# Kernel tuning notes

Measured on AMD Instinct MI355X. Metric: run time of the kernel, lower is better.

## Reference

```python
import jax, jax.numpy as jnp
import numpy as np

B, S, D = 2, 2048, 3584
H, KV, HD = 28, 4, 128
N_REP = H // KV          # 7
MAX_S = 2048
SCALE = HD ** -0.5
ROPE_BASE = 1_000_000.0  # Qwen2 rope theta


def _rope_tables(max_s, hd, base):
    inv = 1.0 / (base ** (np.arange(0, hd, 2, dtype=np.float32) / hd))  # [hd/2]
    ang = np.arange(max_s, dtype=np.float32)[:, None] * inv[None, :]    # [S, hd/2]
    return jnp.asarray(np.cos(ang)), jnp.asarray(np.sin(ang))


def apply_rotary(x, cos, sin):
    # x: [b, s, h, hd] with interleaved complex pairs (torch view_as_complex layout)
    xr = x[..., 0::2]
    xi = x[..., 1::2]
    cos = cos[None, :, None, :]
    sin = sin[None, :, None, :]
    yr = xr * cos - xi * sin
    yi = xr * sin + xi * cos
    return jnp.stack([yr, yi], axis=-1).reshape(x.shape)


def setup_inputs() -> dict:
    key = jax.random.key(0)
    ks = jax.random.split(key, 8)
    w = 0.02
    x = jax.random.normal(ks[0], (B, S, D), jnp.float32)
    wq_w = jax.random.normal(ks[1], (H * HD, D), jnp.float32) * w
    wq_b = jax.random.normal(ks[2], (H * HD,), jnp.float32) * w
    wk_w = jax.random.normal(ks[3], (KV * HD, D), jnp.float32) * w
    wk_b = jax.random.normal(ks[4], (KV * HD,), jnp.float32) * w
    wv_w = jax.random.normal(ks[5], (KV * HD, D), jnp.float32) * w
    wv_b = jax.random.normal(ks[6], (KV * HD,), jnp.float32) * w
    wo_w = jax.random.normal(ks[7], (D, H * HD), jnp.float32) * w
    k_cache = jnp.zeros((B, MAX_S, KV, HD), jnp.float32)
    v_cache = jnp.zeros((B, MAX_S, KV, HD), jnp.float32)
    freqs_cos, freqs_sin = _rope_tables(MAX_S, HD, ROPE_BASE)
    # causal additive mask [s, t]; large-negative instead of -inf for safe grads
    mask = jnp.triu(jnp.full((S, S), -1e9, jnp.float32), k=1)
    return {"x": x, "wq_w": wq_w, "wq_b": wq_b, "wk_w": wk_w, "wk_b": wk_b,
            "wv_w": wv_w, "wv_b": wv_b, "wo_w": wo_w,
            "k_cache": k_cache, "v_cache": v_cache,
            "freqs_cos": freqs_cos, "freqs_sin": freqs_sin,
            "mask": mask, "start_pos": 0}


def reference(x, wq_w, wq_b, wk_w, wk_b, wv_w, wv_b, wo_w,
              k_cache, v_cache, freqs_cos, freqs_sin, mask, start_pos):
    bsz, seqlen, _ = x.shape
    end_pos = start_pos + seqlen
    q = (x @ wq_w.T + wq_b).reshape(bsz, seqlen, H, HD)
    k = (x @ wk_w.T + wk_b).reshape(bsz, seqlen, KV, HD)
    v = (x @ wv_w.T + wv_b).reshape(bsz, seqlen, KV, HD)
    cos = jax.lax.dynamic_slice_in_dim(freqs_cos, start_pos, seqlen, 0)
    sin = jax.lax.dynamic_slice_in_dim(freqs_sin, start_pos, seqlen, 0)
    q = apply_rotary(q, cos, sin)
    k = apply_rotary(k, cos, sin)
    # KV-cache write
    k_cache = jax.lax.dynamic_update_slice(k_cache, k, (0, start_pos, 0, 0))
    v_cache = jax.lax.dynamic_update_slice(v_cache, v, (0, start_pos, 0, 0))
    keys = k_cache[:bsz, :end_pos]    # [b, t, kv, hd]
    values = v_cache[:bsz, :end_pos]
    # GQA: repeat_interleave kv heads to n_heads
    keys = jnp.repeat(keys, N_REP, axis=2)      # [b, t, h, hd]
    values = jnp.repeat(values, N_REP, axis=2)
    scores = jnp.einsum('bshd,bthd->bsht', q, keys) * SCALE
    scores = scores + mask[None, :, None, :]
    probs = jax.nn.softmax(scores.astype(jnp.float32), axis=-1).astype(x.dtype)
    out = jnp.einsum('bsht,bthd->bshd', probs, values)
    out = out.reshape(bsz, seqlen, H * HD)
    return out @ wo_w.T
```

## Files before the change

kernel.cpp:

```cpp
#include <hip/hip_runtime.h>
#include <hip/hip_bf16.h>

typedef __attribute__((ext_vector_type(4)))  float  f32x4;
typedef __attribute__((ext_vector_type(16))) float  f32x16;
typedef __attribute__((ext_vector_type(8)))  __bf16 bf16x8;
typedef __attribute__((ext_vector_type(4)))  __bf16 bf16x4;
typedef __attribute__((ext_vector_type(4)))  unsigned int u32x4;

constexpr int S_LEN = 2048, DMODEL = 3584, NH = 28, NKV = 4, HD = 128, NREP = 7;
constexpr float SCALE_LOG2 = 0.1275174331f;

__device__ __forceinline__ unsigned int pack2(float a, float b) {
  unsigned short ua = __builtin_bit_cast(unsigned short, (__bf16)a);
  unsigned short ub = __builtin_bit_cast(unsigned short, (__bf16)b);
  return (unsigned int)ua | ((unsigned int)ub << 16);
}

__global__ void cvt5_kernel(const float* __restrict__ s0, const float* __restrict__ s1,
                            const float* __restrict__ s2, const float* __restrict__ s3,
                            const float* __restrict__ s4,
                            __bf16* __restrict__ d0, __bf16* __restrict__ d1,
                            __bf16* __restrict__ d2, __bf16* __restrict__ d3,
                            __bf16* __restrict__ d4,
                            int n0, int n1, int n2, int n3, int* __restrict__ ctr, int total) {
  if (blockIdx.x == 0 && threadIdx.x == 0) *ctr = 0;
  for (int i = blockIdx.x * blockDim.x + threadIdx.x; i < total; i += gridDim.x * blockDim.x) {
    const float* s; __bf16* d; int j = i;
    if (j < n0) { s = s0; d = d0; }
    else { j -= n0;
      if (j < n1) { s = s1; d = d1; }
      else { j -= n1;
        if (j < n2) { s = s2; d = d2; }
        else { j -= n2;
          if (j < n3) { s = s3; d = d3; }
          else { j -= n3; s = s4; d = d4; }
        }
      }
    }
    float4 v = reinterpret_cast<const float4*>(s)[j];
    bf16x4 o;
    o[0] = (__bf16)v.x; o[1] = (__bf16)v.y; o[2] = (__bf16)v.z; o[3] = (__bf16)v.w;
    reinterpret_cast<bf16x4*>(d)[j] = o;
  }
}

#define GLDS16(gsrc, ldst)                                                              \
  __builtin_amdgcn_global_load_lds((const __attribute__((address_space(1))) void*)(gsrc),\
                                   (__attribute__((address_space(3))) void*)(ldst), 16, 0, 0)

template <int MODE>
__global__ __launch_bounds__(512, 2) void gemm256(
    const __bf16* __restrict__ A, const __bf16* __restrict__ Bw,
    const float* __restrict__ bias, void* __restrict__ Cout,
    int M, int N, int K,
    const float* __restrict__ fcos, const float* __restrict__ fsin,
    const int* __restrict__ sp_ptr, float scale)
{
  extern __shared__ char smem[];
  const int tid = threadIdx.x;
  const int lane = tid & 63, wid = tid >> 6;
  const int wm = wid >> 2, wn = wid & 3;
  const int l15 = lane & 15, g = (lane >> 4) & 3;

  const int chunk = gridDim.x >> 3;
  const int wg = (blockIdx.x & 7) * chunk + (blockIdx.x >> 3);
  const int nbx = N >> 8;
  const int by = wg / nbx, bx = wg % nbx;
  const int row0 = by * 256, col0 = bx * 256;

  const int srL   = 16 * (tid >> 6) + ((tid >> 2) & 15);
  const int cperm = ((tid & 3) * 8) ^ (((tid >> 5) & 1) * 16);
  const __bf16* pA0 = A + (size_t)(row0 + srL) * K + cperm;
  const __bf16* pA1 = pA0 + (size_t)128 * K;
  const __bf16* pB0 = Bw + (size_t)(col0 + srL) * K + cperm;
  const __bf16* pB1 = pB0 + (size_t)128 * K;
  char* ldsA = smem + tid * 16;
  char* ldsB = smem + 65536 + tid * 16;

  const int sw = ((l15 >> 3) & 1) << 5;
  const int aoff = wm * 8192 + l15 * 64 + ((g * 16) ^ sw);
  const int boff = 65536 + wn * 4096 + l15 * 64 + ((g * 16) ^ sw);

  f32x4 acc[8][4] = {};
  const int nt = K >> 5;

#pragma unroll
  for (int pt = 0; pt < 3; pt++) {
    const size_t ko = (size_t)pt * 32;
    char* sA = ldsA + pt * 16384;
    char* sB = ldsB + pt * 16384;
    GLDS16(pA0 + ko, sA);
    GLDS16(pA1 + ko, sA + 8192);
    GLDS16(pB0 + ko, sB);
    GLDS16(pB1 + ko, sB + 8192);
  }
  asm volatile("s_waitcnt vmcnt(8)" ::: "memory");
  __builtin_amdgcn_s_barrier();
  __builtin_amdgcn_sched_barrier(0);

  for (int t = 0; t < nt; t++) {
    const int slot = (t & 3) * 16384;
    const char* sa = smem + slot + aoff;
    const char* sb = smem + slot + boff;
    bf16x8 a0[4], a1[4], bfv[4];

#pragma unroll
    for (int fn = 0; fn < 4; fn++)
      bfv[fn] = *reinterpret_cast<const bf16x8*>(sb + fn * 1024);
#pragma unroll
    for (int fm = 0; fm < 4; fm++)
      a0[fm] = *reinterpret_cast<const bf16x8*>(sa + fm * 1024);
#pragma unroll
    for (int fm = 0; fm < 4; fm++)
      a1[fm] = *reinterpret_cast<const bf16x8*>(sa + (4 + fm) * 1024);

    if (t + 3 < nt) {
      const size_t ko = (size_t)(t + 3) * 32;
      char* sA = ldsA + ((t + 3) & 3) * 16384;
      char* sB = ldsB + ((t + 3) & 3) * 16384;
      GLDS16(pA0 + ko, sA);
      GLDS16(pA1 + ko, sA + 8192);
      GLDS16(pB0 + ko, sB);
      GLDS16(pB1 + ko, sB + 8192);
    }

    asm volatile("s_waitcnt lgkmcnt(4)" ::: "memory");
    __builtin_amdgcn_sched_barrier(0);
    __builtin_amdgcn_s_setprio(1);
#pragma unroll
    for (int fn = 0; fn < 4; fn++)
#pragma unroll
      for (int fm = 0; fm < 4; fm++)
        acc[fm][fn] = __builtin_amdgcn_mfma_f32_16x16x32_bf16(a0[fm], bfv[fn], acc[fm][fn], 0, 0, 0);
    __builtin_amdgcn_s_setprio(0);

    asm volatile("s_waitcnt lgkmcnt(0)" ::: "memory");
    __builtin_amdgcn_sched_barrier(0);
    __builtin_amdgcn_s_setprio(1);
#pragma unroll
    for (int fn = 0; fn < 4; fn++)
#pragma unroll
      for (int fm = 0; fm < 4; fm++)
        acc[4 + fm][fn] = __builtin_amdgcn_mfma_f32_16x16x32_bf16(a1[fm], bfv[fn], acc[4 + fm][fn], 0, 0, 0);
    __builtin_amdgcn_s_setprio(0);

    if (t < nt - 3)       asm volatile("s_waitcnt vmcnt(8)" ::: "memory");
    else if (t == nt - 3) asm volatile("s_waitcnt vmcnt(4)" ::: "memory");
    else if (t == nt - 2) asm volatile("s_waitcnt vmcnt(0)" ::: "memory");
    __builtin_amdgcn_s_barrier();
    __builtin_amdgcn_sched_barrier(0);
  }

  if constexpr (MODE == 0) {
    float* C = (float*)Cout;
#pragma unroll
    for (int fm = 0; fm < 8; fm++) {
      const int row = row0 + wm * 128 + fm * 16 + 4 * g;
#pragma unroll
      for (int fn = 0; fn < 4; fn++) {
        const int col = col0 + wn * 64 + fn * 16 + l15;
#pragma unroll
        for (int r = 0; r < 4; r++)
          C[(size_t)(row + r) * N + col] = acc[fm][fn][r];
      }
    }
  } else {
    __bf16* C = (__bf16*)Cout;
    const int sp = sp_ptr[0];
    float bval[4];
#pragma unroll
    for (int fn = 0; fn < 4; fn++) bval[fn] = bias[col0 + wn * 64 + fn * 16 + l15];
#pragma unroll
    for (int fm = 0; fm < 8; fm++) {
#pragma unroll
      for (int fn = 0; fn < 4; fn++) {
        const int col = col0 + wn * 64 + fn * 16 + l15;
        const int i = (col & (HD - 1)) >> 1;
#pragma unroll
        for (int r = 0; r < 4; r++) {
          const int row = row0 + wm * 128 + fm * 16 + 4 * g + r;
          float y = acc[fm][fn][r] + bval[fn];
          float p = __shfl_xor(y, 1);
          const int spos = sp + (row & (S_LEN - 1));
          const float c = fcos[spos * (HD / 2) + i];
          const float sn = fsin[spos * (HD / 2) + i];
          y = (col & 1) ? (p * sn + y * c) : (y * c - p * sn);
          C[(size_t)row * N + col] = (__bf16)(y * scale);
        }
      }
    }
  }
}

__global__ __launch_bounds__(256) void gemm_kv(
    const __bf16* __restrict__ A,
    const __bf16* __restrict__ Wk, const float* __restrict__ bk, __bf16* __restrict__ Ko,
    const __bf16* __restrict__ Wv, const float* __restrict__ bv, __bf16* __restrict__ Vo,
    const float* __restrict__ fcos, const float* __restrict__ fsin,
    const int* __restrict__ sp_ptr)
{
  constexpr int N = 512, K = 3584;
  __shared__ __bf16 As[128 * 32];
  __shared__ __bf16 Bs[128 * 32];
  const int tid = threadIdx.x;
  const int lane = tid & 63, wid = tid >> 6;
  const int l15 = lane & 15, g = lane >> 4;
  const int wr = wid >> 1, wc = wid & 1;
  const bool isK = blockIdx.x < 4;
  const __bf16* Bw = isK ? Wk : Wv;
  const float* bias = isK ? bk : bv;
  __bf16* Cout = isK ? Ko : Vo;
  const int row0 = blockIdx.y * 128;
  const int col0 = (blockIdx.x & 3) * 128;

  f32x4 acc[4][4] = {};

  const int srow = tid >> 2;
  const int scol = (tid & 3) * 8;
  const __bf16* Ag0 = A + (size_t)(row0 + srow) * K + scol;
  const __bf16* Ag1 = Ag0 + (size_t)64 * K;
  const __bf16* Bg0 = Bw + (size_t)(col0 + srow) * K + scol;
  const __bf16* Bg1 = Bg0 + (size_t)64 * K;
  __bf16* As0 = As + tid * 8;
  __bf16* As1 = As + 2048 + tid * 8;
  __bf16* Bs0 = Bs + tid * 8;
  __bf16* Bs1 = Bs + 2048 + tid * 8;

  for (int k0 = 0; k0 < K; k0 += 32) {
    GLDS16(Ag0 + k0, As0);
    GLDS16(Ag1 + k0, As1);
    GLDS16(Bg0 + k0, Bs0);
    GLDS16(Bg1 + k0, Bs1);
    __syncthreads();
    bf16x8 af[4], bfr[4];
#pragma unroll
    for (int m = 0; m < 4; m++)
      af[m] = *reinterpret_cast<const bf16x8*>(As + (wr * 64 + m * 16 + l15) * 32 + g * 8);
#pragma unroll
    for (int n = 0; n < 4; n++)
      bfr[n] = *reinterpret_cast<const bf16x8*>(Bs + (wc * 64 + n * 16 + l15) * 32 + g * 8);
#pragma unroll
    for (int m = 0; m < 4; m++)
#pragma unroll
      for (int n = 0; n < 4; n++)
        acc[m][n] = __builtin_amdgcn_mfma_f32_16x16x32_bf16(af[m], bfr[n], acc[m][n], 0, 0, 0);
    __syncthreads();
  }

  const int sp = sp_ptr[0];
#pragma unroll
  for (int m = 0; m < 4; m++) {
#pragma unroll
    for (int n = 0; n < 4; n++) {
      const int col = col0 + wc * 64 + n * 16 + l15;
      const float bval = bias[col];
      f32x4 v = acc[m][n];
#pragma unroll
      for (int r = 0; r < 4; r++) {
        const int row = row0 + wr * 64 + m * 16 + 4 * g + r;
        float y = v[r] + bval;
        if (isK) {
          float p = __shfl_xor(y, 1);
          const int i = (col & (HD - 1)) >> 1;
          const int spos = sp + (row & (S_LEN - 1));
          const float c = fcos[spos * (HD / 2) + i];
          const float sn = fsin[spos * (HD / 2) + i];
          y = (col & 1) ? (p * sn + y * c) : (y * c - p * sn);
        }
        Cout[(size_t)row * N + col] = (__bf16)y;
      }
    }
  }
}

__global__ void vtrans_kernel(const __bf16* __restrict__ Vg, __bf16* __restrict__ Vt) {
  __shared__ __bf16 t[32][33];
  const int bkv = blockIdx.z;
  const int b = bkv >> 2, kv = bkv & 3;
  const int s0 = blockIdx.x * 32, h0 = blockIdx.y * 32;
  const int tid = threadIdx.x;
#pragma unroll
  for (int c = 0; c < 4; c++) {
    int idx = c * 256 + tid;
    int sr = idx >> 5, hc = idx & 31;
    t[sr][hc] = Vg[(((size_t)b * S_LEN + s0 + sr) * NKV + kv) * HD + h0 + hc];
  }
  __syncthreads();
#pragma unroll
  for (int c = 0; c < 4; c++) {
    int idx = c * 256 + tid;
    int hr = idx >> 5, sc = idx & 31;
    Vt[(((size_t)b * NKV + kv) * HD + h0 + hr) * S_LEN + s0 + sc] = t[sc][hr];
  }
}

__global__ __launch_bounds__(256, 2) void attn_kernel(
    const __bf16* __restrict__ Qb, const __bf16* __restrict__ Kb,
    const __bf16* __restrict__ Vt, __bf16* __restrict__ Ob, int* __restrict__ ctr)
{
  __shared__ __align__(16) char asmem[65536];
  __shared__ int jsh;

  const int tid = threadIdx.x, lane = tid & 63, wid = tid >> 6;
  const int l31 = lane & 31, hh = lane >> 5;

  const int trow = tid >> 4;
  const int kcol = (((tid & 15) * 16) ^ ((trow & 7) << 4)) >> 1;
  const int vrow = tid >> 3;
  const int vcol = (((tid & 7) * 16) ^ ((vrow & 7) << 4)) >> 1;

  constexpr int NITEMS = 16 * NH * 2;

  while (true) {
    if (tid == 0) jsh = atomicAdd(ctr, 1);
    __syncthreads();
    const int j = jsh;
    if (j >= NITEMS) break;

    const int qi = 15 - (j / 56);
    const int r56 = j % 56;
    const int h = r56 >> 1, b = r56 & 1;
    const int kvh = h / NREP;
    const int qw = qi * 128 + wid * 32;
    const int qg = qw + l31;

    const __bf16* Kbase = Kb + ((size_t)b * S_LEN * NKV + kvh) * HD;
    const __bf16* Vbase = Vt + ((size_t)b * NKV + kvh) * (size_t)HD * S_LEN;

    bf16x8 qf[8];
    {
      const __bf16* qp = Qb + (((size_t)b * S_LEN + qg) * NH + h) * HD + hh * 8;
#pragma unroll
      for (int c = 0; c < 8; c++) qf[c] = *reinterpret_cast<const bf16x8*>(qp + c * 16);
    }

    f32x16 o[4] = {};
    float mrun = -3.0e38f, lsum = 0.0f;

    const int ntiles = 2 * qi + 2;

#define STAGE(T, S)                                                                     \
    do {                                                                                \
      const int k0_ = (T) * 64;                                                         \
      char* Kd_ = asmem + (S) * 32768;                                                  \
      char* Vd_ = Kd_ + 16384;                                                          \
      _Pragma("unroll")                                                                 \
      for (int p = 0; p < 4; p++) {                                                     \
        GLDS16(Kbase + (size_t)(k0_ + p * 16 + trow) * (NKV * HD) + kcol,               \
               Kd_ + (p * 256 + tid) * 16);                                             \
        GLDS16(Vbase + (size_t)(p * 32 + vrow) * S_LEN + k0_ + vcol,                    \
               Vd_ + (p * 256 + tid) * 16);                                             \
      }                                                                                 \
    } while (0)

    STAGE(0, 0);

    for (int t = 0; t < ntiles; t++) {
      __syncthreads();
      if (t + 1 < ntiles) STAGE(t + 1, (t + 1) & 1);

      const char* Ksb = asmem + (t & 1) * 32768;
      const char* Vsb = Ksb + 16384;
      const int k0 = t * 64;

      f32x16 s0 = {}, s1 = {};
      {
        const char* kp0 = Ksb + l31 * 256;
        const char* kp1 = kp0 + 32 * 256;
        const int sw = (l31 & 7) << 4;
        __builtin_amdgcn_s_setprio(1);
#pragma unroll
        for (int c = 0; c < 8; c++) {
          const int cb = (c * 32 + hh * 16) ^ sw;
          bf16x8 kf0 = *reinterpret_cast<const bf16x8*>(kp0 + cb);
          s0 = __builtin_amdgcn_mfma_f32_32x32x16_bf16(kf0, qf[c], s0, 0, 0, 0);
          bf16x8 kf1 = *reinterpret_cast<const bf16x8*>(kp1 + cb);
          s1 = __builtin_amdgcn_mfma_f32_32x32x16_bf16(kf1, qf[c], s1, 0, 0, 0);
        }
        __builtin_amdgcn_s_setprio(0);
      }

      if (k0 + 63 > qw) {
#pragma unroll
        for (int r = 0; r < 16; r++) {
          const int kvo = k0 + ((r & 3) + 8 * (r >> 2)) + 4 * hh;
          if (kvo > qg)      s0[r] = -1.0e9f;
          if (kvo + 32 > qg) s1[r] = -1.0e9f;
        }
      }

      float pmax = -3.0e38f;
#pragma unroll
      for (int r = 0; r < 16; r++) { pmax = fmaxf(pmax, s0[r]); pmax = fmaxf(pmax, s1[r]); }
      pmax = fmaxf(pmax, __shfl_xor(pmax, 32));
      if (!__all(pmax <= mrun + 11.5f)) {
        const float mnew = fmaxf(mrun, pmax);
        const float fs = exp2f(mrun - mnew);
        lsum *= fs;
#pragma unroll
        for (int dt = 0; dt < 4; dt++) o[dt] *= fs;
        mrun = mnew;
      }
      float psum = 0.0f;
#pragma unroll
      for (int r = 0; r < 16; r++) {
        s0[r] = exp2f(s0[r] - mrun); psum += s0[r];
        s1[r] = exp2f(s1[r] - mrun); psum += s1[r];
      }
      lsum += psum;

      unsigned int pk[2][8], px[2][8];
#pragma unroll
      for (int jj = 0; jj < 8; jj++) {
        pk[0][jj] = pack2(s0[2 * jj], s0[2 * jj + 1]);
        pk[1][jj] = pack2(s1[2 * jj], s1[2 * jj + 1]);
      }
#pragma unroll
      for (int tt = 0; tt < 2; tt++)
#pragma unroll
        for (int jj = 0; jj < 8; jj++) px[tt][jj] = __shfl_xor(pk[tt][jj], 32);

      __builtin_amdgcn_s_setprio(1);
#pragma unroll
      for (int tt = 0; tt < 2; tt++) {
#pragma unroll
        for (int c2 = 0; c2 < 2; c2++) {
          u32x4 pb4;
          if (hh == 0)
            pb4 = (u32x4){pk[tt][4 * c2], pk[tt][4 * c2 + 1], px[tt][4 * c2], px[tt][4 * c2 + 1]};
          else
            pb4 = (u32x4){px[tt][4 * c2 + 2], px[tt][4 * c2 + 3], pk[tt][4 * c2 + 2], pk[tt][4 * c2 + 3]};
          bf16x8 pbf = __builtin_bit_cast(bf16x8, pb4);
          const int colb = tt * 64 + c2 * 32 + hh * 16;
#pragma unroll
          for (int dt = 0; dt < 4; dt++) {
            const int d = dt * 32 + l31;
            bf16x8 vf = *reinterpret_cast<const bf16x8*>(Vsb + d * 128 + (colb ^ ((d & 7) << 4)));
            o[dt] = __builtin_amdgcn_mfma_f32_32x32x16_bf16(vf, pbf, o[dt], 0, 0, 0);
          }
        }
      }
      __builtin_amdgcn_s_setprio(0);
    }
#undef STAGE

    lsum += __shfl_xor(lsum, 32);
    const float inv = 1.0f / lsum;
    char* my = asmem + wid * 8192;
#pragma unroll
    for (int dt = 0; dt < 4; dt++) {
#pragma unroll
      for (int jj = 0; jj < 8; jj++) {
        const int r = 2 * jj;
        const int d = dt * 32 + ((r & 3) + 8 * (r >> 2)) + 4 * hh;
        const unsigned int w = pack2(o[dt][r] * inv, o[dt][r + 1] * inv);
        *reinterpret_cast<unsigned int*>(my + ((l31 * 256 + d * 2) ^ ((l31 & 7) << 4))) = w;
      }
    }
#pragma unroll
    for (int jj = 0; jj < 8; jj++) {
      const int idx = jj * 64 + lane;
      const int row = idx >> 4, c16 = idx & 15;
      u32x4 val = *reinterpret_cast<u32x4*>(my + row * 256 + ((c16 * 16) ^ ((row & 7) << 4)));
      *reinterpret_cast<u32x4*>(Ob + (size_t)(b * S_LEN + qw + row) * (NH * HD) + h * HD + c16 * 8) = val;
    }
  }
}

extern "C" void kernel_launch(void* const* d_in, const int* in_sizes, int n_in,
                              void* d_out, int out_size, void* d_ws, size_t ws_size,
                              hipStream_t stream) {
  (void)in_sizes; (void)n_in; (void)out_size; (void)ws_size;
  const float* x    = (const float*)d_in[0];
  const float* wq_w = (const float*)d_in[1];
  const float* wq_b = (const float*)d_in[2];
  const float* wk_w = (const float*)d_in[3];
  const float* wk_b = (const float*)d_in[4];
  const float* wv_w = (const float*)d_in[5];
  const float* wv_b = (const float*)d_in[6];
  const float* wo_w = (const float*)d_in[7];
  const float* fcos = (const float*)d_in[10];
  const float* fsin = (const float*)d_in[11];
  const int*   spp  = (const int*)d_in[13];
  float* out = (float*)d_out;

  constexpr size_t XB_N = (size_t)4096 * 3584;
  constexpr size_t WQ_N = (size_t)3584 * 3584;
  constexpr size_t WK_N = (size_t)512 * 3584;
  constexpr size_t WO_N = (size_t)3584 * 3584;
  constexpr size_t KB_N = (size_t)4096 * 512;

  __bf16* xb  = (__bf16*)d_ws;
  __bf16* wqb = xb + XB_N;
  __bf16* wkb = wqb + WQ_N;
  __bf16* wvb = wkb + WK_N;
  __bf16* wob = wvb + WK_N;
  __bf16* Qb  = wob + WO_N;
  __bf16* Kb  = Qb + XB_N;
  __bf16* Vg  = Kb + KB_N;
  __bf16* Vt  = Vg + KB_N;
  int*    ctr = (int*)(Vt + KB_N);
  __bf16* Ob  = xb;

  constexpr int N0 = (int)(XB_N / 4), N1 = (int)(WQ_N / 4), N2 = (int)(WK_N / 4),
                N3 = (int)(WK_N / 4), N4 = (int)(WO_N / 4);
  constexpr int NTOT = N0 + N1 + N2 + N3 + N4;
  cvt5_kernel<<<2048, 256, 0, stream>>>(x, wq_w, wk_w, wv_w, wo_w,
                                        xb, wqb, wkb, wvb, wob,
                                        N0, N1, N2, N3, ctr, NTOT);

  gemm256<2><<<dim3(224), 512, 131072, stream>>>(xb, wqb, wq_b, Qb, 4096, 3584, 3584,
                                                 fcos, fsin, spp, SCALE_LOG2);
  gemm_kv<<<dim3(8, 32), 256, 0, stream>>>(xb, wkb, wk_b, Kb, wvb, wv_b, Vg,
                                           fcos, fsin, spp);
  vtrans_kernel<<<dim3(64, 4, 8), 256, 0, stream>>>(Vg, Vt);
  attn_kernel<<<dim3(512), 256, 0, stream>>>(Qb, Kb, Vt, Ob, ctr);
  gemm256<0><<<dim3(224), 512, 131072, stream>>>(Ob, wob, nullptr, out, 4096, 3584, 3584,
                                                 nullptr, nullptr, nullptr, 1.0f);
}
```

Measured before the change: 432.9 us.

## Use 32x32x16 MFMA in big GEMMs and fuse V transpose into KV GEMM

The 256x256 GEMM tiles move from 16x16x32 MFMA fragments to 32x32x16 fragments with 16-float accumulators, and the LDS read offsets and epilogue row/column mapping are recomputed to match the new layout. Separately, the KV projection kernel now writes V directly in transposed [b,kv,hd,s] form, so the standalone vtrans kernel and the intermediate V buffer are removed. The aim is fewer LDS reads per MFMA and one less launch plus a round trip through memory. The risks are LDS bank conflicts from the new read pattern and strided 8-byte stores in the fused V epilogue.

```diff
diff --git a/kernel.cpp b/kernel.cpp
--- a/kernel.cpp
+++ b/kernel.cpp
@@ -60,7 +60,8 @@
   const int tid = threadIdx.x;
   const int lane = tid & 63, wid = tid >> 6;
   const int wm = wid >> 2, wn = wid & 3;
-  const int l15 = lane & 15, g = (lane >> 4) & 3;
+  const int l31 = lane & 31, hh = lane >> 5;
+  const int l15 = lane & 15;
 
   const int chunk = gridDim.x >> 3;
   const int wg = (blockIdx.x & 7) * chunk + (blockIdx.x >> 3);
@@ -77,11 +78,14 @@
   char* ldsA = smem + tid * 16;
   char* ldsB = smem + 65536 + tid * 16;
 
-  const int sw = ((l15 >> 3) & 1) << 5;
-  const int aoff = wm * 8192 + l15 * 64 + ((g * 16) ^ sw);
-  const int boff = 65536 + wn * 4096 + l15 * 64 + ((g * 16) ^ sw);
-
-  f32x4 acc[8][4] = {};
+  const int laneoff = (l31 >> 4) * 1024 + l15 * 64 + hh * 16;
+  const int ksx = (l31 & 8) << 2;
+  const int abase = wm * 8192 + laneoff;
+  const int R0 = wn * 64, R1 = wn * 64 + 32;
+  const int bo0 = (R0 >> 7) * 8192 + ((R0 >> 4) & 7) * 1024;
+  const int bo1 = (R1 >> 7) * 8192 + ((R1 >> 4) & 7) * 1024;
+
+  f32x16 acc[4][2] = {};
   const int nt = K >> 5;
 
 #pragma unroll
@@ -100,19 +104,21 @@
 
   for (int t = 0; t < nt; t++) {
     const int slot = (t & 3) * 16384;
-    const char* sa = smem + slot + aoff;
-    const char* sb = smem + slot + boff;
-    bf16x8 a0[4], a1[4], bfv[4];
-
-#pragma unroll
-    for (int fn = 0; fn < 4; fn++)
-      bfv[fn] = *reinterpret_cast<const bf16x8*>(sb + fn * 1024);
+    const char* sa = smem + slot + abase;
+    const char* sb = smem + slot + 65536 + laneoff;
+    bf16x8 a0[4], a1[4], b0[2], b1[2];
+
+    b0[0] = *reinterpret_cast<const bf16x8*>(sb + bo0 + ksx);
+    b0[1] = *reinterpret_cast<const bf16x8*>(sb + bo1 + ksx);
 #pragma unroll
     for (int fm = 0; fm < 4; fm++)
-      a0[fm] = *reinterpret_cast<const bf16x8*>(sa + fm * 1024);
+      a0[fm] = *reinterpret_cast<const bf16x8*>(sa + fm * 2048 + ksx);
+    __builtin_amdgcn_sched_barrier(0);
+    b1[0] = *reinterpret_cast<const bf16x8*>(sb + bo0 + (32 ^ ksx));
+    b1[1] = *reinterpret_cast<const bf16x8*>(sb + bo1 + (32 ^ ksx));
 #pragma unroll
     for (int fm = 0; fm < 4; fm++)
-      a1[fm] = *reinterpret_cast<const bf16x8*>(sa + (4 + fm) * 1024);
+      a1[fm] = *reinterpret_cast<const bf16x8*>(sa + fm * 2048 + (32 ^ ksx));
 
     if (t + 3 < nt) {
       const size_t ko = (size_t)(t + 3) * 32;
@@ -124,24 +130,24 @@
       GLDS16(pB1 + ko, sB + 8192);
     }
 
-    asm volatile("s_waitcnt lgkmcnt(4)" ::: "memory");
+    asm volatile("s_waitcnt lgkmcnt(6)" ::: "memory");
     __builtin_amdgcn_sched_barrier(0);
     __builtin_amdgcn_s_setprio(1);
 #pragma unroll
-    for (int fn = 0; fn < 4; fn++)
+    for (int fn = 0; fn < 2; fn++)
 #pragma unroll
       for (int fm = 0; fm < 4; fm++)
-        acc[fm][fn] = __builtin_amdgcn_mfma_f32_16x16x32_bf16(a0[fm], bfv[fn], acc[fm][fn], 0, 0, 0);
+        acc[fm][fn] = __builtin_amdgcn_mfma_f32_32x32x16_bf16(a0[fm], b0[fn], acc[fm][fn], 0, 0, 0);
     __builtin_amdgcn_s_setprio(0);
 
     asm volatile("s_waitcnt lgkmcnt(0)" ::: "memory");
     __builtin_amdgcn_sched_barrier(0);
     __builtin_amdgcn_s_setprio(1);
 #pragma unroll
-    for (int fn = 0; fn < 4; fn++)
+    for (int fn = 0; fn < 2; fn++)
 #pragma unroll
       for (int fm = 0; fm < 4; fm++)
-        acc[4 + fm][fn] = __builtin_amdgcn_mfma_f32_16x16x32_bf16(a1[fm], bfv[fn], acc[4 + fm][fn], 0, 0, 0);
+        acc[fm][fn] = __builtin_amdgcn_mfma_f32_32x32x16_bf16(a1[fm], b1[fn], acc[fm][fn], 0, 0, 0);
     __builtin_amdgcn_s_setprio(0);
 
     if (t < nt - 3)       asm volatile("s_waitcnt vmcnt(8)" ::: "memory");
@@ -154,31 +160,32 @@
   if constexpr (MODE == 0) {
     float* C = (float*)Cout;
 #pragma unroll
-    for (int fm = 0; fm < 8; fm++) {
-      const int row = row0 + wm * 128 + fm * 16 + 4 * g;
-#pragma unroll
-      for (int fn = 0; fn < 4; fn++) {
-        const int col = col0 + wn * 64 + fn * 16 + l15;
-#pragma unroll
-        for (int r = 0; r < 4; r++)
-          C[(size_t)(row + r) * N + col] = acc[fm][fn][r];
+    for (int fm = 0; fm < 4; fm++) {
+#pragma unroll
+      for (int fn = 0; fn < 2; fn++) {
+        const int col = col0 + wn * 64 + fn * 32 + l31;
+#pragma unroll
+        for (int r = 0; r < 16; r++) {
+          const int row = row0 + wm * 128 + fm * 32 + (r & 3) + 8 * (r >> 2) + 4 * hh;
+          C[(size_t)row * N + col] = acc[fm][fn][r];
+        }
       }
     }
   } else {
     __bf16* C = (__bf16*)Cout;
     const int sp = sp_ptr[0];
-    float bval[4];
-#pragma unroll
-    for (int fn = 0; fn < 4; fn++) bval[fn] = bias[col0 + wn * 64 + fn * 16 + l15];
-#pragma unroll
-    for (int fm = 0; fm < 8; fm++) {
-#pragma unroll
-      for (int fn = 0; fn < 4; fn++) {
-        const int col = col0 + wn * 64 + fn * 16 + l15;
+    float bval[2];
+#pragma unroll
+    for (int fn = 0; fn < 2; fn++) bval[fn] = bias[col0 + wn * 64 + fn * 32 + l31];
+#pragma unroll
+    for (int fm = 0; fm < 4; fm++) {
+#pragma unroll
+      for (int fn = 0; fn < 2; fn++) {
+        const int col = col0 + wn * 64 + fn * 32 + l31;
         const int i = (col & (HD - 1)) >> 1;
 #pragma unroll
-        for (int r = 0; r < 4; r++) {
-          const int row = row0 + wm * 128 + fm * 16 + 4 * g + r;
+        for (int r = 0; r < 16; r++) {
+          const int row = row0 + wm * 128 + fm * 32 + (r & 3) + 8 * (r >> 2) + 4 * hh;
           float y = acc[fm][fn][r] + bval[fn];
           float p = __shfl_xor(y, 1);
           const int spos = sp + (row & (S_LEN - 1));
@@ -195,7 +202,7 @@
 __global__ __launch_bounds__(256) void gemm_kv(
     const __bf16* __restrict__ A,
     const __bf16* __restrict__ Wk, const float* __restrict__ bk, __bf16* __restrict__ Ko,
-    const __bf16* __restrict__ Wv, const float* __restrict__ bv, __bf16* __restrict__ Vo,
+    const __bf16* __restrict__ Wv, const float* __restrict__ bv, __bf16* __restrict__ Vt,
     const float* __restrict__ fcos, const float* __restrict__ fsin,
     const int* __restrict__ sp_ptr)
 {
@@ -209,7 +216,6 @@
   const bool isK = blockIdx.x < 4;
   const __bf16* Bw = isK ? Wk : Wv;
   const float* bias = isK ? bk : bv;
-  __bf16* Cout = isK ? Ko : Vo;
   const int row0 = blockIdx.y * 128;
   const int col0 = (blockIdx.x & 3) * 128;
 
@@ -248,49 +254,45 @@
   }
 
   const int sp = sp_ptr[0];
-#pragma unroll
-  for (int m = 0; m < 4; m++) {
-#pragma unroll
-    for (int n = 0; n < 4; n++) {
-      const int col = col0 + wc * 64 + n * 16 + l15;
-      const float bval = bias[col];
-      f32x4 v = acc[m][n];
-#pragma unroll
-      for (int r = 0; r < 4; r++) {
-        const int row = row0 + wr * 64 + m * 16 + 4 * g + r;
-        float y = v[r] + bval;
-        if (isK) {
+  if (isK) {
+#pragma unroll
+    for (int m = 0; m < 4; m++) {
+#pragma unroll
+      for (int n = 0; n < 4; n++) {
+        const int col = col0 + wc * 64 + n * 16 + l15;
+        const float bval = bias[col];
+        f32x4 v = acc[m][n];
+#pragma unroll
+        for (int r = 0; r < 4; r++) {
+          const int row = row0 + wr * 64 + m * 16 + 4 * g + r;
+          float y = v[r] + bval;
           float p = __shfl_xor(y, 1);
           const int i = (col & (HD - 1)) >> 1;
           const int spos = sp + (row & (S_LEN - 1));
           const float c = fcos[spos * (HD / 2) + i];
           const float sn = fsin[spos * (HD / 2) + i];
           y = (col & 1) ? (p * sn + y * c) : (y * c - p * sn);
-        }
-        Cout[(size_t)row * N + col] = (__bf16)y;
-      }
-    }
-  }
-}
-
-__global__ void vtrans_kernel(const __bf16* __restrict__ Vg, __bf16* __restrict__ Vt) {
-  __shared__ __bf16 t[32][33];
-  const int bkv = blockIdx.z;
-  const int b = bkv >> 2, kv = bkv & 3;
-  const int s0 = blockIdx.x * 32, h0 = blockIdx.y * 32;
-  const int tid = threadIdx.x;
-#pragma unroll
-  for (int c = 0; c < 4; c++) {
-    int idx = c * 256 + tid;
-    int sr = idx >> 5, hc = idx & 31;
-    t[sr][hc] = Vg[(((size_t)b * S_LEN + s0 + sr) * NKV + kv) * HD + h0 + hc];
-  }
-  __syncthreads();
-#pragma unroll
-  for (int c = 0; c < 4; c++) {
-    int idx = c * 256 + tid;
-    int hr = idx >> 5, sc = idx & 31;
-    Vt[(((size_t)b * NKV + kv) * HD + h0 + hr) * S_LEN + s0 + sc] = t[sc][hr];
+          Ko[(size_t)row * N + col] = (__bf16)y;
+        }
+      }
+    }
+  } else {
+    const int b4kv = ((row0 >> 11) * 4) + (blockIdx.x & 3);
+    __bf16* vbase = Vt + ((size_t)b4kv << 18);
+#pragma unroll
+    for (int m = 0; m < 4; m++) {
+#pragma unroll
+      for (int n = 0; n < 4; n++) {
+        const int d = wc * 64 + n * 16 + l15;
+        const float bval = bias[col0 + d];
+        const int s0 = (row0 + wr * 64 + m * 16 + 4 * g) & (S_LEN - 1);
+        f32x4 v = acc[m][n];
+        bf16x4 o;
+#pragma unroll
+        for (int r = 0; r < 4; r++) o[r] = (__bf16)(v[r] + bval);
+        *reinterpret_cast<bf16x4*>(vbase + (size_t)d * S_LEN + s0) = o;
+      }
+    }
   }
 }
 
@@ -497,8 +499,7 @@
   __bf16* wob = wvb + WK_N;
   __bf16* Qb  = wob + WO_N;
   __bf16* Kb  = Qb + XB_N;
-  __bf16* Vg  = Kb + KB_N;
-  __bf16* Vt  = Vg + KB_N;
+  __bf16* Vt  = Kb + KB_N;
   int*    ctr = (int*)(Vt + KB_N);
   __bf16* Ob  = xb;
 
@@ -511,9 +512,8 @@
 
   gemm256<2><<<dim3(224), 512, 131072, stream>>>(xb, wqb, wq_b, Qb, 4096, 3584, 3584,
                                                  fcos, fsin, spp, SCALE_LOG2);
-  gemm_kv<<<dim3(8, 32), 256, 0, stream>>>(xb, wkb, wk_b, Kb, wvb, wv_b, Vg,
+  gemm_kv<<<dim3(8, 32), 256, 0, stream>>>(xb, wkb, wk_b, Kb, wvb, wv_b, Vt,
                                            fcos, fsin, spp);
-  vtrans_kernel<<<dim3(64, 4, 8), 256, 0, stream>>>(Vg, Vt);
   attn_kernel<<<dim3(512), 256, 0, stream>>>(Qb, Kb, Vt, Ob, ctr);
   gemm256<0><<<dim3(224), 512, 131072, stream>>>(Ob, wob, nullptr, out, 4096, 3584, 3584,
                                                  nullptr, nullptr, nullptr, 1.0f);
```

Result: slower. 443.7 us (+2.5%).
